# Optimization experiments

Measured on AMD Instinct MI355X. Metric: run time of the kernel, lower is better.

Reference implementation:

```python
import jax, jax.numpy as jnp
import numpy as np

D_MODEL = 1024
N_HEADS = 16
HEAD_DIM = D_MODEL // N_HEADS
NEG_INF = -1e9


def setup_inputs() -> dict:
    key = jax.random.key(0)
    ks = jax.random.split(key, 12)
    B, S = 2, 2048
    std = 1.0 / np.sqrt(D_MODEL)
    def lin(k):
        kw, kb = jax.random.split(k)
        W = jax.random.uniform(kw, (D_MODEL, D_MODEL), jnp.float32, -std, std)
        b = jax.random.uniform(kb, (D_MODEL,), jnp.float32, -std, std)
        return W, b
    Wq, bq = lin(ks[0])
    Wk, bk = lin(ks[1])
    Wv, bv = lin(ks[2])
    Wo, bo = lin(ks[3])
    Q = jax.random.normal(ks[4], (B, S, D_MODEL), jnp.float32)
    K = jax.random.normal(ks[5], (B, S, D_MODEL), jnp.float32)
    V = jax.random.normal(ks[6], (B, S, D_MODEL), jnp.float32)
    # causal attention mask: True means masked (disallowed)
    attn_mask = jnp.triu(jnp.ones((S, S), dtype=bool), k=1)
    padding_mask = jnp.zeros((B, S), dtype=bool)  # no padding
    return {"Q": Q, "K": K, "V": V, "attn_mask": attn_mask,
            "padding_mask": padding_mask,
            "Wq": Wq, "bq": bq, "Wk": Wk, "bk": bk,
            "Wv": Wv, "bv": bv, "Wo": Wo, "bo": bo}


def reference(Q, K, V, attn_mask, padding_mask, Wq, bq, Wk, bk, Wv, bv, Wo, bo):
    B, Sq, _ = Q.shape
    Sk = K.shape[1]
    # QKV projections, split into heads -> [B, H, S, Dh]
    def proj(x, W, b):
        y = x @ W.T + b
        return y.reshape(B, -1, N_HEADS, HEAD_DIM).transpose(0, 2, 1, 3)
    q = proj(Q, Wq, bq)
    k = proj(K, Wk, bk)
    v = proj(V, Wv, bv)
    # scaled dot-product attention (dropout is identity in eval mode)
    scores = jnp.einsum('bhqd,bhkd->bhqk', q, k) / jnp.sqrt(
        jnp.asarray(HEAD_DIM, q.dtype))
    mask = attn_mask[None, None, :, :] | padding_mask[:, None, None, :]
    scores = jnp.where(mask, NEG_INF, scores)
    attn = jax.nn.softmax(scores, axis=-1)
    x = jnp.einsum('bhqk,bhkd->bhqd', attn, v)
    x = x.transpose(0, 2, 1, 3).reshape(B, Sq, D_MODEL)
    return x @ Wo.T + bo
```

## Files before the change

### kernel.cpp

```cpp
#include <hip/hip_runtime.h>
#include <hip/hip_bf16.h>
#include <cstddef>
#include <cstdint>

#define S_LEN  2048
#define DMODEL 1024
#define NHEADS 16

typedef __attribute__((ext_vector_type(8))) short  short8;
typedef __attribute__((ext_vector_type(4))) short  s16x4;
typedef __attribute__((ext_vector_type(8))) __bf16 bf16x8;
typedef __attribute__((ext_vector_type(4))) float  f32x4;

__device__ __forceinline__ f32x4 MFMA(short8 a, short8 b, f32x4 c) {
    return __builtin_amdgcn_mfma_f32_16x16x32_bf16(
        __builtin_bit_cast(bf16x8, a), __builtin_bit_cast(bf16x8, b), c, 0, 0, 0);
}

__device__ __forceinline__ unsigned short f2bs(float f) {
    return __builtin_bit_cast(unsigned short, __float2bfloat16(f));
}
__device__ __forceinline__ float bs2f(unsigned short u) {
    unsigned int x = ((unsigned int)u) << 16;
    return __builtin_bit_cast(float, x);
}

__device__ __forceinline__ short8 cvt8(f32x4 a, f32x4 b) {
    short8 r;
#pragma unroll
    for (int i = 0; i < 4; ++i) {
        r[i]     = (short)f2bs(a[i]);
        r[4 + i] = (short)f2bs(b[i]);
    }
    return r;
}

__device__ __forceinline__ short8 scale8(short8 v) {
    short8 r;
#pragma unroll
    for (int i = 0; i < 8; ++i)
        r[i] = (short)f2bs(bs2f((unsigned short)v[i]) * 0.125f);
    return r;
}

__device__ __forceinline__ int xcd_swz(int bid, int nwg) {
    const int chunk = nwg >> 3;
    return (bid & 7) * chunk + (bid >> 3);
}

__device__ __forceinline__ void bar_sync() {
    asm volatile("s_waitcnt lgkmcnt(0)" ::: "memory");
    __builtin_amdgcn_sched_barrier(0);
    __builtin_amdgcn_s_barrier();
}

template<bool HEADSPLIT>
__device__ __forceinline__ void gemm_body(const void* __restrict__ Ap,
                                          const float* __restrict__ W,
                                          const float* __restrict__ bias,
                                          void* __restrict__ outp,
                                          int m0, int n0)
{
    __shared__ short a_lds[2][128 * 32];
    __shared__ short w_lds[2][128 * 32];
    const int t    = threadIdx.x;
    const int lane = t & 63;
    const int wid  = t >> 6;
    const int wr   = (wid >> 1) << 6;
    const int wc   = (wid & 1) << 6;
    const int fr   = lane & 15;
    const int ks   = lane >> 4;

    const int row0 = t >> 2,         sl0 = t & 3;
    const int row1 = (256 + t) >> 2, sl1 = (256 + t) & 3;
    const int ms0  = sl0 ^ ((row0 >> 1) & 3);
    const int ms1  = sl1 ^ ((row1 >> 1) & 3);

    short8 av_b[2];
    f32x4  av_f[2][2];
    f32x4  wv_f[2][2];

    auto load_tile = [&](int k0) {
        if constexpr (HEADSPLIT) {
            const float* A = (const float*)Ap;
            const float* pa0 = A + (size_t)(m0 + row0) * DMODEL + k0 + sl0 * 8;
            av_f[0][0] = ((const f32x4*)pa0)[0]; av_f[0][1] = ((const f32x4*)pa0)[1];
            const float* pa1 = A + (size_t)(m0 + row1) * DMODEL + k0 + sl1 * 8;
            av_f[1][0] = ((const f32x4*)pa1)[0]; av_f[1][1] = ((const f32x4*)pa1)[1];
        } else {
            const unsigned short* A = (const unsigned short*)Ap;
            av_b[0] = *(const short8*)(A + (size_t)(m0 + row0) * DMODEL + k0 + sl0 * 8);
            av_b[1] = *(const short8*)(A + (size_t)(m0 + row1) * DMODEL + k0 + sl1 * 8);
        }
        const float* pw0 = W + (size_t)(n0 + row0) * DMODEL + k0 + sl0 * 8;
        wv_f[0][0] = ((const f32x4*)pw0)[0]; wv_f[0][1] = ((const f32x4*)pw0)[1];
        const float* pw1 = W + (size_t)(n0 + row1) * DMODEL + k0 + sl1 * 8;
        wv_f[1][0] = ((const f32x4*)pw1)[0]; wv_f[1][1] = ((const f32x4*)pw1)[1];
    };

    auto store_tile = [&](int buf) {
        if constexpr (HEADSPLIT) {
            *(short8*)&a_lds[buf][row0 * 32 + ms0 * 8] = cvt8(av_f[0][0], av_f[0][1]);
            *(short8*)&a_lds[buf][row1 * 32 + ms1 * 8] = cvt8(av_f[1][0], av_f[1][1]);
        } else {
            *(short8*)&a_lds[buf][row0 * 32 + ms0 * 8] = av_b[0];
            *(short8*)&a_lds[buf][row1 * 32 + ms1 * 8] = av_b[1];
        }
        *(short8*)&w_lds[buf][row0 * 32 + ms0 * 8] = cvt8(wv_f[0][0], wv_f[0][1]);
        *(short8*)&w_lds[buf][row1 * 32 + ms1 * 8] = cvt8(wv_f[1][0], wv_f[1][1]);
    };

    load_tile(0);
    store_tile(0);
    load_tile(32);
    bar_sync();

    f32x4 acc[4][4] = {};

    for (int kidx = 0; kidx < 32; ++kidx) {
        const int cur = kidx & 1;

        short8 af[4], bfr[4];
#pragma unroll
        for (int i = 0; i < 4; ++i) {
            const int ra = wr + i * 16 + fr;
            af[i]  = *(const short8*)&a_lds[cur][ra * 32 + ((ks ^ ((ra >> 1) & 3)) << 3)];
            const int rb = wc + i * 16 + fr;
            bfr[i] = *(const short8*)&w_lds[cur][rb * 32 + ((ks ^ ((rb >> 1) & 3)) << 3)];
        }
#pragma unroll
        for (int mi = 0; mi < 4; ++mi)
#pragma unroll
            for (int ni = 0; ni < 4; ++ni)
                acc[mi][ni] = MFMA(af[mi], bfr[ni], acc[mi][ni]);

        if (kidx + 1 < 32) {
            store_tile(cur ^ 1);
            if (kidx + 2 < 32) load_tile((kidx + 2) * 32);
        }
        bar_sync();
    }

#pragma unroll
    for (int ni = 0; ni < 4; ++ni) {
        const int n    = n0 + wc + ni * 16 + fr;
        const float bv = bias[n];
#pragma unroll
        for (int mi = 0; mi < 4; ++mi) {
#pragma unroll
            for (int j = 0; j < 4; ++j) {
                const int m = m0 + wr + mi * 16 + ks * 4 + j;
                const float val = acc[mi][ni][j] + bv;
                if constexpr (HEADSPLIT) {
                    const int b = m >> 11, s = m & (S_LEN - 1);
                    const int hh = n >> 6, dh = n & 63;
                    ((unsigned short*)outp)[((((size_t)b * NHEADS + hh) * S_LEN + s) << 6) + dh]
                        = f2bs(val);
                } else {
                    ((float*)outp)[(size_t)m * DMODEL + n] = val;
                }
            }
        }
    }
}

__global__ __launch_bounds__(256, 3)
void qkv_gemm(const float* __restrict__ Q, const float* __restrict__ K,
              const float* __restrict__ V,
              const float* __restrict__ Wq, const float* __restrict__ Wk,
              const float* __restrict__ Wv,
              const float* __restrict__ bq, const float* __restrict__ bk,
              const float* __restrict__ bv,
              unsigned short* qh, unsigned short* kh, unsigned short* vh)
{
    const int swz = xcd_swz(blockIdx.x, 768);
    const int z   = swz >> 8;
    const int rem = swz & 255;
    const int my  = rem >> 3;
    const int nx  = rem & 7;
    const float *A, *W, *B; unsigned short* O;
    if (z == 0)      { A = Q; W = Wq; B = bq; O = qh; }
    else if (z == 1) { A = K; W = Wk; B = bk; O = kh; }
    else             { A = V; W = Wv; B = bv; O = vh; }
    gemm_body<true>(A, W, B, O, my * 128, nx * 128);
}

__global__ __launch_bounds__(256, 3)
void out_gemm(const unsigned short* __restrict__ X, const float* __restrict__ Wo,
              const float* __restrict__ bo, float* __restrict__ out)
{
    const int swz = xcd_swz(blockIdx.x, 256);
    gemm_body<false>(X, Wo, bo, out, (swz >> 3) * 128, (swz & 7) * 128);
}

#define VSTR 72
#define PSTR 88

struct QState {
    short8 qf0, qf1;
    f32x4  oacc[4];
    float  m, l;
    int    qr0;
};

__device__ __forceinline__ void attn_tile(QState& st, const int k0,
                                          const short* k_lds, const short* v_lds,
                                          short* p_buf, const int fr, const int ks)
{
    const int myq = st.qr0 + fr;
    f32x4 sacc[4] = {};
    __builtin_amdgcn_s_setprio(1);
#pragma unroll
    for (int nk = 0; nk < 4; ++nk) {
        const int rb = nk * 16 + fr;
        short8 a0 = *(const short8*)&k_lds[rb * 64 + (((ks)     ^ (rb & 7)) << 3)];
        short8 a1 = *(const short8*)&k_lds[rb * 64 + (((4 + ks) ^ (rb & 7)) << 3)];
        sacc[nk] = MFMA(a0, st.qf0, sacc[nk]);
        sacc[nk] = MFMA(a1, st.qf1, sacc[nk]);
    }
    __builtin_amdgcn_s_setprio(0);

    float mx = -1e9f;
    if (k0 + 63 <= st.qr0) {
#pragma unroll
        for (int nk = 0; nk < 4; ++nk)
#pragma unroll
            for (int jj = 0; jj < 4; ++jj) mx = fmaxf(mx, sacc[nk][jj]);
    } else {
#pragma unroll
        for (int nk = 0; nk < 4; ++nk)
#pragma unroll
            for (int jj = 0; jj < 4; ++jj) {
                const int key = k0 + nk * 16 + ks * 4 + jj;
                float s = (key <= myq) ? sacc[nk][jj] : -1e9f;
                sacc[nk][jj] = s;
                mx = fmaxf(mx, s);
            }
    }
    mx = fmaxf(mx, __shfl_xor(mx, 16));
    mx = fmaxf(mx, __shfl_xor(mx, 32));
    if (!__all(mx <= st.m + 8.f)) {
        const float mnew = fmaxf(st.m, mx);
        const float corr = __expf(st.m - mnew);
        st.m = mnew;
        st.l *= corr;
#pragma unroll
        for (int nd = 0; nd < 4; ++nd)
#pragma unroll
            for (int jj = 0; jj < 4; ++jj) st.oacc[nd][jj] *= corr;
    }

    float rsum = 0.f;
#pragma unroll
    for (int nk = 0; nk < 4; ++nk) {
        s16x4 pw;
#pragma unroll
        for (int jj = 0; jj < 4; ++jj) {
            const float p = __expf(sacc[nk][jj] - st.m);
            rsum += p;
            pw[jj] = (short)f2bs(p);
        }
        *(s16x4*)&p_buf[fr * PSTR + nk * 16 + ks * 4] = pw;
    }
    rsum += __shfl_xor(rsum, 16);
    rsum += __shfl_xor(rsum, 32);
    st.l += rsum;
    asm volatile("" ::: "memory");

    __builtin_amdgcn_s_setprio(1);
#pragma unroll
    for (int sh = 0; sh < 2; ++sh) {
        short8 pa = *(const short8*)&p_buf[fr * PSTR + sh * 32 + ks * 8];
#pragma unroll
        for (int nd = 0; nd < 4; ++nd) {
            short8 vf = *(const short8*)&v_lds[(nd * 16 + fr) * VSTR + sh * 32 + ks * 8];
            st.oacc[nd] = MFMA(vf, pa, st.oacc[nd]);
        }
    }
    __builtin_amdgcn_s_setprio(0);
}

__global__ __launch_bounds__(256, 2)
void attn_kernel(const unsigned short* __restrict__ qh,
                 const unsigned short* __restrict__ kh,
                 const unsigned short* __restrict__ vh,
                 unsigned short* __restrict__ xh)
{
    __shared__ short k_lds[64 * 64];
    __shared__ short v_lds[64 * VSTR];
    __shared__ short p_lds[4][16 * PSTR];

    const int t    = threadIdx.x;
    const int lane = t & 63;
    const int wid  = t >> 6;
    const int fr   = lane & 15;
    const int ks   = lane >> 4;
    const int swz  = xcd_swz(blockIdx.x, 512);
    const int bh   = swz >> 4;
    const int xp   = swz & 15;
    const int qa0  = xp * 64;
    const int qb0  = (31 - xp) * 64;
    const int ntA  = xp + 1;
    const int ntB  = 32 - xp;

    const unsigned short* qb_ = qh + ((size_t)bh << 17);
    const unsigned short* kb  = kh + ((size_t)bh << 17);
    const unsigned short* vb  = vh + ((size_t)bh << 17);

    QState A, B;
    A.qr0 = qa0 + wid * 16;  B.qr0 = qb0 + wid * 16;
    A.qf0 = scale8(*(const short8*)&qb_[(A.qr0 + fr) * 64 + ks * 8]);
    A.qf1 = scale8(*(const short8*)&qb_[(A.qr0 + fr) * 64 + 32 + ks * 8]);
    B.qf0 = scale8(*(const short8*)&qb_[(B.qr0 + fr) * 64 + ks * 8]);
    B.qf1 = scale8(*(const short8*)&qb_[(B.qr0 + fr) * 64 + 32 + ks * 8]);
#pragma unroll
    for (int nd = 0; nd < 4; ++nd) { A.oacc[nd] = f32x4{}; B.oacc[nd] = f32x4{}; }
    A.m = B.m = -1e9f; A.l = B.l = 0.f;

    short8 kv[2], vv[2];
#pragma unroll
    for (int cc = 0; cc < 2; ++cc) {
        const int c   = cc * 256 + t;
        const int row = c >> 3;
        const int sl  = c & 7;
        kv[cc] = *(const short8*)(kb + (size_t)row * 64 + sl * 8);
        const int key = c & 63;
        const int d0  = (c >> 6) * 8;
        vv[cc] = *(const short8*)(vb + (size_t)key * 64 + d0);
    }

    for (int kt = 0; kt < ntB; ++kt) {
        const int k0 = kt * 64;
        bar_sync();

#pragma unroll
        for (int cc = 0; cc < 2; ++cc) {
            const int c   = cc * 256 + t;
            const int row = c >> 3;
            const int ms  = (c & 7) ^ (row & 7);
            *(short8*)&k_lds[row * 64 + ms * 8] = kv[cc];
            const int key = c & 63;
            const int d0  = (c >> 6) * 8;
#pragma unroll
            for (int i = 0; i < 8; ++i)
                v_lds[(d0 + i) * VSTR + key] = vv[cc][i];
        }
        bar_sync();

        if (kt + 1 < ntB) {
            const int k1 = k0 + 64;
#pragma unroll
            for (int cc = 0; cc < 2; ++cc) {
                const int c   = cc * 256 + t;
                const int row = c >> 3;
                const int sl  = c & 7;
                kv[cc] = *(const short8*)(kb + (size_t)(k1 + row) * 64 + sl * 8);
                const int key = c & 63;
                const int d0  = (c >> 6) * 8;
                vv[cc] = *(const short8*)(vb + (size_t)(k1 + key) * 64 + d0);
            }
        }

        attn_tile(B, k0, k_lds, v_lds, p_lds[wid], fr, ks);
        if (kt < ntA)
            attn_tile(A, k0, k_lds, v_lds, p_lds[wid], fr, ks);
    }

    const int b = bh >> 4, h = bh & 15;
#pragma unroll
    for (int which = 0; which < 2; ++which) {
        QState& st = which ? B : A;
        const float inv = 1.f / st.l;
        const size_t base = ((size_t)b * S_LEN + (st.qr0 + fr)) * DMODEL + h * 64;
#pragma unroll
        for (int nd = 0; nd < 4; ++nd)
#pragma unroll
            for (int jj = 0; jj < 4; ++jj)
                xh[base + nd * 16 + ks * 4 + jj] = f2bs(st.oacc[nd][jj] * inv);
    }
}

extern "C" void kernel_launch(void* const* d_in, const int* in_sizes, int n_in,
                              void* d_out, int out_size, void* d_ws, size_t ws_size,
                              hipStream_t stream)
{
    const float* Q  = (const float*)d_in[0];
    const float* K  = (const float*)d_in[1];
    const float* V  = (const float*)d_in[2];
    const float* Wq = (const float*)d_in[5];
    const float* bq = (const float*)d_in[6];
    const float* Wk = (const float*)d_in[7];
    const float* bk = (const float*)d_in[8];
    const float* Wv = (const float*)d_in[9];
    const float* bv = (const float*)d_in[10];
    const float* Wo = (const float*)d_in[11];
    const float* bo = (const float*)d_in[12];
    float* out = (float*)d_out;

    const size_t HSZ = (size_t)2 * S_LEN * DMODEL;
    unsigned short* qh = (unsigned short*)d_ws;
    unsigned short* kh = qh + HSZ;
    unsigned short* vh = kh + HSZ;
    unsigned short* xh = vh + HSZ;

    qkv_gemm<<<768, 256, 0, stream>>>(Q, K, V, Wq, Wk, Wv, bq, bk, bv, qh, kh, vh);
    attn_kernel<<<512, 256, 0, stream>>>(qh, kh, vh, xh);
    out_gemm<<<256, 256, 0, stream>>>(xh, Wo, bo, out);
}
```

Measured before the change: 109.0 us.

## Pre-convert QKV weights to bf16 and double-buffer GEMM register stages

A new kernel converts Wq, Wk and Wv to bf16 once per call into workspace that aliases the attention output buffer, so the QKV GEMM loads half as many weight bytes and skips per-tile weight conversion. The GEMM main loop is also unrolled by two with two register staging sets, issuing the next global load before compute to hide latency. The cost is an extra kernel launch plus a full weight read and write pass, and higher register pressure that may affect occupancy at launch bounds of 3.

```diff
diff --git a/kernel.cpp b/kernel.cpp
--- a/kernel.cpp
+++ b/kernel.cpp
@@ -54,9 +54,28 @@
     __builtin_amdgcn_s_barrier();
 }
 
-template<bool HEADSPLIT>
+__global__ __launch_bounds__(256)
+void wcvt(const float* __restrict__ Wq, const float* __restrict__ Wk,
+          const float* __restrict__ Wv, unsigned short* __restrict__ wb)
+{
+    const int i = blockIdx.x * 256 + threadIdx.x;
+    const float* src = (i < 131072) ? Wq : (i < 262144) ? Wk : Wv;
+    const size_t j = (size_t)(i & 131071) * 8;
+    const short8 v = cvt8(((const f32x4*)(src + j))[0], ((const f32x4*)(src + j))[1]);
+    *(short8*)(wb + (size_t)i * 8) = v;
+}
+
+template<bool HEADSPLIT, bool WBF16>
+struct StageRegs {
+    f32x4  af[2][2];
+    short8 ab[2];
+    f32x4  wf[2][2];
+    short8 wb[2];
+};
+
+template<bool HEADSPLIT, bool WBF16>
 __device__ __forceinline__ void gemm_body(const void* __restrict__ Ap,
-                                          const float* __restrict__ W,
+                                          const void* __restrict__ Wp,
                                           const float* __restrict__ bias,
                                           void* __restrict__ outp,
                                           int m0, int n0)
@@ -76,50 +95,54 @@
     const int ms0  = sl0 ^ ((row0 >> 1) & 3);
     const int ms1  = sl1 ^ ((row1 >> 1) & 3);
 
-    short8 av_b[2];
-    f32x4  av_f[2][2];
-    f32x4  wv_f[2][2];
-
-    auto load_tile = [&](int k0) {
+    using SR = StageRegs<HEADSPLIT, WBF16>;
+    SR S0, S1;
+
+    auto load_stage = [&](SR& S, int k0) {
         if constexpr (HEADSPLIT) {
             const float* A = (const float*)Ap;
             const float* pa0 = A + (size_t)(m0 + row0) * DMODEL + k0 + sl0 * 8;
-            av_f[0][0] = ((const f32x4*)pa0)[0]; av_f[0][1] = ((const f32x4*)pa0)[1];
+            S.af[0][0] = ((const f32x4*)pa0)[0]; S.af[0][1] = ((const f32x4*)pa0)[1];
             const float* pa1 = A + (size_t)(m0 + row1) * DMODEL + k0 + sl1 * 8;
-            av_f[1][0] = ((const f32x4*)pa1)[0]; av_f[1][1] = ((const f32x4*)pa1)[1];
+            S.af[1][0] = ((const f32x4*)pa1)[0]; S.af[1][1] = ((const f32x4*)pa1)[1];
         } else {
             const unsigned short* A = (const unsigned short*)Ap;
-            av_b[0] = *(const short8*)(A + (size_t)(m0 + row0) * DMODEL + k0 + sl0 * 8);
-            av_b[1] = *(const short8*)(A + (size_t)(m0 + row1) * DMODEL + k0 + sl1 * 8);
-        }
-        const float* pw0 = W + (size_t)(n0 + row0) * DMODEL + k0 + sl0 * 8;
-        wv_f[0][0] = ((const f32x4*)pw0)[0]; wv_f[0][1] = ((const f32x4*)pw0)[1];
-        const float* pw1 = W + (size_t)(n0 + row1) * DMODEL + k0 + sl1 * 8;
-        wv_f[1][0] = ((const f32x4*)pw1)[0]; wv_f[1][1] = ((const f32x4*)pw1)[1];
+            S.ab[0] = *(const short8*)(A + (size_t)(m0 + row0) * DMODEL + k0 + sl0 * 8);
+            S.ab[1] = *(const short8*)(A + (size_t)(m0 + row1) * DMODEL + k0 + sl1 * 8);
+        }
+        if constexpr (WBF16) {
+            const unsigned short* Wb = (const unsigned short*)Wp;
+            S.wb[0] = *(const short8*)(Wb + (size_t)(n0 + row0) * DMODEL + k0 + sl0 * 8);
+            S.wb[1] = *(const short8*)(Wb + (size_t)(n0 + row1) * DMODEL + k0 + sl1 * 8);
+        } else {
+            const float* W = (const float*)Wp;
+            const float* pw0 = W + (size_t)(n0 + row0) * DMODEL + k0 + sl0 * 8;
+            S.wf[0][0] = ((const f32x4*)pw0)[0]; S.wf[0][1] = ((const f32x4*)pw0)[1];
+            const float* pw1 = W + (size_t)(n0 + row1) * DMODEL + k0 + sl1 * 8;
+            S.wf[1][0] = ((const f32x4*)pw1)[0]; S.wf[1][1] = ((const f32x4*)pw1)[1];
+        }
     };
 
-    auto store_tile = [&](int buf) {
+    auto store_stage = [&](const SR& S, int buf) {
         if constexpr (HEADSPLIT) {
-            *(short8*)&a_lds[buf][row0 * 32 + ms0 * 8] = cvt8(av_f[0][0], av_f[0][1]);
-            *(short8*)&a_lds[buf][row1 * 32 + ms1 * 8] = cvt8(av_f[1][0], av_f[1][1]);
+            *(short8*)&a_lds[buf][row0 * 32 + ms0 * 8] = cvt8(S.af[0][0], S.af[0][1]);
+            *(short8*)&a_lds[buf][row1 * 32 + ms1 * 8] = cvt8(S.af[1][0], S.af[1][1]);
         } else {
-            *(short8*)&a_lds[buf][row0 * 32 + ms0 * 8] = av_b[0];
-            *(short8*)&a_lds[buf][row1 * 32 + ms1 * 8] = av_b[1];
-        }
-        *(short8*)&w_lds[buf][row0 * 32 + ms0 * 8] = cvt8(wv_f[0][0], wv_f[0][1]);
-        *(short8*)&w_lds[buf][row1 * 32 + ms1 * 8] = cvt8(wv_f[1][0], wv_f[1][1]);
+            *(short8*)&a_lds[buf][row0 * 32 + ms0 * 8] = S.ab[0];
+            *(short8*)&a_lds[buf][row1 * 32 + ms1 * 8] = S.ab[1];
+        }
+        if constexpr (WBF16) {
+            *(short8*)&w_lds[buf][row0 * 32 + ms0 * 8] = S.wb[0];
+            *(short8*)&w_lds[buf][row1 * 32 + ms1 * 8] = S.wb[1];
+        } else {
+            *(short8*)&w_lds[buf][row0 * 32 + ms0 * 8] = cvt8(S.wf[0][0], S.wf[0][1]);
+            *(short8*)&w_lds[buf][row1 * 32 + ms1 * 8] = cvt8(S.wf[1][0], S.wf[1][1]);
+        }
     };
 
-    load_tile(0);
-    store_tile(0);
-    load_tile(32);
-    bar_sync();
-
     f32x4 acc[4][4] = {};
 
-    for (int kidx = 0; kidx < 32; ++kidx) {
-        const int cur = kidx & 1;
-
+    auto compute = [&](int cur) {
         short8 af[4], bfr[4];
 #pragma unroll
         for (int i = 0; i < 4; ++i) {
@@ -133,12 +156,22 @@
 #pragma unroll
             for (int ni = 0; ni < 4; ++ni)
                 acc[mi][ni] = MFMA(af[mi], bfr[ni], acc[mi][ni]);
-
-        if (kidx + 1 < 32) {
-            store_tile(cur ^ 1);
-            if (kidx + 2 < 32) load_tile((kidx + 2) * 32);
-        }
+    };
+
+    load_stage(S0, 0);
+    store_stage(S0, 0);
+    load_stage(S1, 32);
+    bar_sync();
+
+    for (int tt = 0; tt < 32; tt += 2) {
+        if (tt + 2 < 32) load_stage(S0, (tt + 2) * 32);
+        compute(0);
+        if (tt + 1 < 32) store_stage(S1, 1);
         bar_sync();
+        if (tt + 3 < 32) load_stage(S1, (tt + 3) * 32);
+        compute(1);
+        if (tt + 2 < 32) store_stage(S0, 0);
+        if (tt + 2 < 32) bar_sync();
     }
 
 #pragma unroll
@@ -167,8 +200,7 @@
 __global__ __launch_bounds__(256, 3)
 void qkv_gemm(const float* __restrict__ Q, const float* __restrict__ K,
               const float* __restrict__ V,
-              const float* __restrict__ Wq, const float* __restrict__ Wk,
-              const float* __restrict__ Wv,
+              const unsigned short* __restrict__ wb,
               const float* __restrict__ bq, const float* __restrict__ bk,
               const float* __restrict__ bv,
               unsigned short* qh, unsigned short* kh, unsigned short* vh)
@@ -178,11 +210,11 @@
     const int rem = swz & 255;
     const int my  = rem >> 3;
     const int nx  = rem & 7;
-    const float *A, *W, *B; unsigned short* O;
-    if (z == 0)      { A = Q; W = Wq; B = bq; O = qh; }
-    else if (z == 1) { A = K; W = Wk; B = bk; O = kh; }
-    else             { A = V; W = Wv; B = bv; O = vh; }
-    gemm_body<true>(A, W, B, O, my * 128, nx * 128);
+    const float *A, *B; unsigned short* O;
+    if (z == 0)      { A = Q; B = bq; O = qh; }
+    else if (z == 1) { A = K; B = bk; O = kh; }
+    else             { A = V; B = bv; O = vh; }
+    gemm_body<true, true>(A, wb + ((size_t)z << 20), B, O, my * 128, nx * 128);
 }
 
 __global__ __launch_bounds__(256, 3)
@@ -190,7 +222,7 @@
               const float* __restrict__ bo, float* __restrict__ out)
 {
     const int swz = xcd_swz(blockIdx.x, 256);
-    gemm_body<false>(X, Wo, bo, out, (swz >> 3) * 128, (swz & 7) * 128);
+    gemm_body<false, false>(X, Wo, bo, out, (swz >> 3) * 128, (swz & 7) * 128);
 }
 
 #define VSTR 72
@@ -402,8 +434,10 @@
     unsigned short* kh = qh + HSZ;
     unsigned short* vh = kh + HSZ;
     unsigned short* xh = vh + HSZ;
-
-    qkv_gemm<<<768, 256, 0, stream>>>(Q, K, V, Wq, Wk, Wv, bq, bk, bv, qh, kh, vh);
+    unsigned short* wb = xh;
+
+    wcvt<<<1536, 256, 0, stream>>>(Wq, Wk, Wv, wb);
+    qkv_gemm<<<768, 256, 0, stream>>>(Q, K, V, wb, bq, bk, bv, qh, kh, vh);
     attn_kernel<<<512, 256, 0, stream>>>(qh, kh, vh, xh);
     out_gemm<<<256, 256, 0, stream>>>(xh, Wo, bo, out);
 }
```

Result: slower. 123.0 us (+12.9%).
